# Kernel tuning notes

Hardware: AMD Instinct MI355X
Metric: run time of the kernel (lower is better)

Reference implementation:

```python
import jax, jax.numpy as jnp
import numpy as np

D_MODEL = 1024
NHEAD = 16
HEAD_DIM = D_MODEL // NHEAD
WINDOW = 256


def setup_inputs() -> dict:
    key = jax.random.key(0)
    kx, kq, kk, kv, ko = jax.random.split(key, 5)
    B, S = 2, 2048
    scale = 1.0 / np.sqrt(D_MODEL)
    x = jax.random.normal(kx, (B, S, D_MODEL), dtype=jnp.float32)
    Wq = jax.random.normal(kq, (D_MODEL, D_MODEL), dtype=jnp.float32) * scale
    Wk = jax.random.normal(kk, (D_MODEL, D_MODEL), dtype=jnp.float32) * scale
    Wv = jax.random.normal(kv, (D_MODEL, D_MODEL), dtype=jnp.float32) * scale
    Wo = jax.random.normal(ko, (D_MODEL, D_MODEL), dtype=jnp.float32) * scale
    return {"x": x, "Wq": Wq, "Wk": Wk, "Wv": Wv, "Wo": Wo}


def _sliding_window_mask(seq_len):
    # additive mask: 0 where (q - window + 1) <= k <= q, -inf elsewhere
    pos = jnp.arange(seq_len)
    qpos = pos[:, None]
    kpos = pos[None, :]
    valid = (kpos >= qpos - WINDOW + 1) & (kpos <= qpos)
    return jnp.where(valid, 0.0, -jnp.inf).astype(jnp.float32)


def reference(x, Wq, Wk, Wv, Wo):
    B, S, D = x.shape
    # projections (nn.Linear: x @ W.T; weights here stored as [out,in] equiv -> use x @ W.T)
    q = jnp.einsum('bsd,ed->bse', x, Wq)
    k = jnp.einsum('bsd,ed->bse', x, Wk)
    v = jnp.einsum('bsd,ed->bse', x, Wv)
    q = q.reshape(B, S, NHEAD, HEAD_DIM).transpose(0, 2, 1, 3)  # [B,H,S,Dh]
    k = k.reshape(B, S, NHEAD, HEAD_DIM).transpose(0, 2, 1, 3)
    v = v.reshape(B, S, NHEAD, HEAD_DIM).transpose(0, 2, 1, 3)
    mask = _sliding_window_mask(S)  # [S,S]
    scale = 1.0 / np.sqrt(HEAD_DIM)
    scores = jnp.einsum('bhqd,bhkd->bhqk', q, k) * scale + mask
    attn = jax.nn.softmax(scores, axis=-1)
    out = jnp.einsum('bhqk,bhkd->bhqd', attn, v)  # [B,H,S,Dh]
    out = out.transpose(0, 2, 1, 3).reshape(B, S, D)
    return jnp.einsum('bsd,ed->bse', out, Wo)
```

## Files before the change

### kernel.cpp

```cpp
#include <hip/hip_runtime.h>
#include <stdint.h>

#define S_LEN   2048
#define BATCH   2
#define DM      1024
#define NHEADS  16
#define HD      64
#define WIN     256
#define MROWS   (BATCH * S_LEN)
#define NX      (MROWS * DM)
#define NW      (DM * DM)

typedef unsigned short u16;
typedef unsigned int   u32;

using short8  = __attribute__((ext_vector_type(8))) short;
using floatx4 = __attribute__((ext_vector_type(4))) float;

__device__ __forceinline__ float bf2f(u16 u) {
    union { u32 u; float f; } v; v.u = ((u32)u) << 16; return v.f;
}
__device__ __forceinline__ u16 f2bf(float f) {
    union { float f; u32 u; } v; v.f = f;
    u32 u = v.u;
    u += 0x7fffu + ((u >> 16) & 1u);
    return (u16)(u >> 16);
}

__device__ __forceinline__ void load_lds16(const void* g, void* l) {
    __builtin_amdgcn_global_load_lds(
        (__attribute__((address_space(1))) void*)(uintptr_t)g,
        (__attribute__((address_space(3))) void*)(unsigned int)(uintptr_t)l,
        16, 0, 0);
}

__global__ __launch_bounds__(256) void normalize_inputs(
        const void* x, const void* wq, const void* wk, const void* wv, const void* wo,
        u16* xb, u16* wcat, u16* wob, int* flag) {
    __shared__ int sbad;
    if (threadIdx.x == 0) sbad = 0;
    __syncthreads();
    int bad = 0;
    for (int i = threadIdx.x; i < 4096; i += 256) {
        float v = bf2f(((const u16*)x)[i]);
        if (!(fabsf(v) < 1e6f)) bad = 1;
    }
    if (bad) atomicOr(&sbad, 1);
    __syncthreads();
    const int mode = sbad;
    if (blockIdx.x == 0 && threadIdx.x == 0) flag[0] = mode;
    if (mode == 0) return;
    const int total4 = (NX + 4 * NW) >> 2;
    for (int i4 = blockIdx.x * blockDim.x + threadIdx.x; i4 < total4;
         i4 += gridDim.x * blockDim.x) {
        const int i = i4 << 2;
        const float* src; u16* dst; int li;
        if (i < NX)              { src = (const float*)x;  dst = xb;          li = i; }
        else if (i < NX + NW)    { src = (const float*)wq; dst = wcat;        li = i - NX; }
        else if (i < NX + 2*NW)  { src = (const float*)wk; dst = wcat + NW;   li = i - NX - NW; }
        else if (i < NX + 3*NW)  { src = (const float*)wv; dst = wcat + 2*NW; li = i - NX - 2*NW; }
        else                     { src = (const float*)wo; dst = wob;         li = i - NX - 3*NW; }
        float4 v = *(const float4*)(src + li);
        ushort4 o;
        o.x = f2bf(v.x); o.y = f2bf(v.y); o.z = f2bf(v.z); o.w = f2bf(v.w);
        *(ushort4*)(dst + li) = o;
    }
}

#define BK 32
#define QSCALE 0.180336880f

template<int TBM, int TBN>
__global__ __launch_bounds__(256) void gemm_lds(
        const u16* __restrict__ Araw, const u16* __restrict__ Anorm,
        const u16* __restrict__ B0, const u16* __restrict__ B1,
        const u16* __restrict__ B2, const u16* __restrict__ Bnorm,
        void* __restrict__ C, u16* __restrict__ VT,
        int M, int N, int K,
        const int* __restrict__ flag, int final_out) {
    constexpr int NI = TBM / 32, NF = TBN / 32;
    __shared__ __align__(16) u16 sA[2][TBM * BK];
    __shared__ __align__(16) u16 sB[2][TBN * BK];

    const int mode = flag[0];
    const int tid  = threadIdx.x;
    const int lane = tid & 63, wave = tid >> 6;
    const int m0  = blockIdx.x * TBM;
    const int n0g = blockIdx.y * TBN;
    const int third = n0g >> 10;
    const u16* A = mode ? Anorm : Araw;
    const u16* B = mode ? (Bnorm + (size_t)third * NW)
                        : (third == 0 ? B0 : (third == 1 ? B1 : B2));
    const int n0 = n0g - third * 1024;

    const int srow = lane >> 2;
    const int scol = (lane & 3) * 8;
    const u16* gA = A + (size_t)(m0 + wave * 16 + srow) * K + scol;
    const u16* gB = B + (size_t)(n0 + wave * 16 + srow) * K + scol;
    const size_t rstep = (size_t)64 * K;
    const int lofs = wave * 16 * BK;

    const int n16 = lane & 15, quad = lane >> 4;
    const int m_off = (wave >> 1) * (TBM / 2), n_off = (wave & 1) * (TBN / 2);

    floatx4 acc[NI][NF] = {};
    const int NIT = K / BK;

    auto issue = [&](int k0, int buf) {
        #pragma unroll
        for (int ia = 0; ia < TBM / 64; ++ia)
            load_lds16(gA + k0 + ia * rstep, sA[buf] + lofs + ia * 64 * BK);
        #pragma unroll
        for (int ib = 0; ib < TBN / 64; ++ib)
            load_lds16(gB + k0 + ib * rstep, sB[buf] + lofs + ib * 64 * BK);
    };

    issue(0, 0);
    for (int it = 0; it < NIT; ++it) {
        const int cur = it & 1;
        __syncthreads();
        if (it + 1 < NIT) issue((it + 1) * BK, 1 - cur);
        short8 af[NI], bfr[NF];
        #pragma unroll
        for (int i = 0; i < NI; ++i)
            af[i] = *(const short8*)&sA[cur][(m_off + i * 16 + n16) * BK + quad * 8];
        #pragma unroll
        for (int j = 0; j < NF; ++j)
            bfr[j] = *(const short8*)&sB[cur][(n_off + j * 16 + n16) * BK + quad * 8];
        #pragma unroll
        for (int i = 0; i < NI; ++i) {
            #pragma unroll
            for (int j = 0; j < NF; ++j)
                acc[i][j] = __builtin_amdgcn_mfma_f32_16x16x32_bf16(
                    af[i], bfr[j], acc[i][j], 0, 0, 0);
        }
    }

    if (!final_out && n0g >= 2048) {
        #pragma unroll
        for (int i = 0; i < NI; ++i) {
            #pragma unroll
            for (int j = 0; j < NF; ++j) {
                int row = m0 + m_off + i * 16 + quad * 4;
                int b_ = row >> 11, s = row & 2047;
                int cv = (n0g - 2048) + n_off + j * 16 + n16;
                int h_ = cv >> 6, dl = cv & 63;
                u16 pack[4];
                #pragma unroll
                for (int r = 0; r < 4; ++r) pack[r] = f2bf(acc[i][j][r]);
                u16* dst = VT + (((size_t)(b_ * 16 + h_) * 64 + dl) * S_LEN + s);
                *(uint2*)dst = *(uint2*)pack;
            }
        }
        return;
    }
    const int outmode = final_out ? mode : 0;
    const float oscale = (!final_out && n0g < 1024) ? QSCALE : 1.0f;
    #pragma unroll
    for (int i = 0; i < NI; ++i) {
        #pragma unroll
        for (int j = 0; j < NF; ++j) {
            #pragma unroll
            for (int r = 0; r < 4; ++r) {
                int row = m0 + m_off + i * 16 + quad * 4 + r;
                int col = n0g + n_off + j * 16 + n16;
                size_t idx = (size_t)row * N + col;
                float v = acc[i][j][r] * oscale;
                if (outmode) ((float*)C)[idx] = v;
                else         ((u16*)C)[idx]   = f2bf(v);
            }
        }
    }
}

__global__ __launch_bounds__(256) void gemm_out(
        const u16* __restrict__ A,
        const u16* __restrict__ Braw,
        const u16* __restrict__ Bnorm,
        void* __restrict__ C,
        const int* __restrict__ flag) {
    __shared__ __align__(16) u16 sA[2][128 * 64];
    __shared__ __align__(16) u16 sB[2][64 * 64];

    const int mode = flag[0];
    const u16* B = mode ? Bnorm : Braw;
    const int tid  = threadIdx.x;
    const int lane = tid & 63, wave = tid >> 6;
    const int n16 = lane & 15, quad = lane >> 4;
    const int m0 = blockIdx.x * 128;
    const int n0 = blockIdx.y * 64;
    const int K = DM;

    const int srow = tid >> 3;
    const int scol = (tid & 7) * 8;
    const u16* gA = A + (size_t)(m0 + srow) * K + scol;
    const u16* gB = B + (size_t)(n0 + srow) * K + scol;
    const int lofs = wave * 512;

    auto issue = [&](int k0, int buf) {
        #pragma unroll
        for (int ia = 0; ia < 4; ++ia)
            load_lds16(gA + k0 + (size_t)ia * 32 * K, sA[buf] + ia * 2048 + lofs);
        #pragma unroll
        for (int ib = 0; ib < 2; ++ib)
            load_lds16(gB + k0 + (size_t)ib * 32 * K, sB[buf] + ib * 2048 + lofs);
    };

    const int m_off = (wave >> 1) * 64, n_off = (wave & 1) * 32;
    floatx4 acc[4][2] = {};

    issue(0, 0);
    for (int it = 0; it < 16; ++it) {
        const int cur = it & 1;
        __syncthreads();
        if (it + 1 < 16) issue((it + 1) * 64, 1 - cur);
        short8 a0[4], a1[4], b0[2], b1[2];
        #pragma unroll
        for (int i = 0; i < 4; ++i) {
            const int rb = (m_off + i * 16 + n16) * 64;
            a0[i] = *(const short8*)&sA[cur][rb + quad * 8];
            a1[i] = *(const short8*)&sA[cur][rb + 32 + quad * 8];
        }
        #pragma unroll
        for (int j = 0; j < 2; ++j) {
            const int rb = (n_off + j * 16 + n16) * 64;
            b0[j] = *(const short8*)&sB[cur][rb + quad * 8];
            b1[j] = *(const short8*)&sB[cur][rb + 32 + quad * 8];
        }
        #pragma unroll
        for (int i = 0; i < 4; ++i) {
            #pragma unroll
            for (int j = 0; j < 2; ++j)
                acc[i][j] = __builtin_amdgcn_mfma_f32_16x16x32_bf16(
                    a0[i], b0[j], acc[i][j], 0, 0, 0);
        }
        #pragma unroll
        for (int i = 0; i < 4; ++i) {
            #pragma unroll
            for (int j = 0; j < 2; ++j)
                acc[i][j] = __builtin_amdgcn_mfma_f32_16x16x32_bf16(
                    a1[i], b1[j], acc[i][j], 0, 0, 0);
        }
    }

    #pragma unroll
    for (int i = 0; i < 4; ++i) {
        #pragma unroll
        for (int j = 0; j < 2; ++j) {
            #pragma unroll
            for (int r = 0; r < 4; ++r) {
                int row = m0 + m_off + i * 16 + quad * 4 + r;
                int col = n0 + n_off + j * 16 + n16;
                size_t idx = (size_t)row * DM + col;
                float v = acc[i][j][r];
                if (mode) ((float*)C)[idx] = v;
                else      ((u16*)C)[idx]   = f2bf(v);
            }
        }
    }
}

#define NCHUNK 10

__global__ __launch_bounds__(256) void attn_mfma(
        const u16* __restrict__ QKV, const u16* __restrict__ VT,
        u16* __restrict__ O) {
    __shared__ __align__(16) u16 sK[2][32][72];
    __shared__ __align__(16) u16 sVt[2][64][40];
    __shared__ __align__(16) u16 sP[4][2][16][40];

    const int bh = blockIdx.x;
    const int b  = bh >> 4, h = bh & 15;
    const int q0 = blockIdx.y * 64;
    const int ks0 = q0 - 256;
    const int tid = threadIdx.x;
    const u16* base = QKV + (size_t)b * S_LEN * 3072;
    const u16* Kb = base + 1024 + h * 64;
    const u16* Vb = VT + (size_t)bh * 64 * S_LEN;

    const int kRow = tid >> 3;
    const int kSeg = tid & 7;
    const int vD   = tid >> 2;
    const int vSeg = tid & 3;

    auto issue_loads = [&](int c, uint4& kv, uint4& vv) {
        const int ks = ks0 + c * 32;
        int kg = ks + kRow;
        uint4 k0 = {0u, 0u, 0u, 0u};
        if (kg >= 0 && kg < S_LEN)
            k0 = *(const uint4*)(Kb + (size_t)kg * 3072 + kSeg * 8);
        kv = k0;
        int vk = ks + vSeg * 8;
        uint4 v0 = {0u, 0u, 0u, 0u};
        if (vk >= 0 && vk + 8 <= S_LEN)
            v0 = *(const uint4*)(Vb + (size_t)vD * S_LEN + vk);
        vv = v0;
    };
    auto write_lds = [&](int buf, const uint4& kv, const uint4& vv) {
        *(uint4*)&sK[buf][kRow][kSeg * 8] = kv;
        *(uint4*)&sVt[buf][vD][vSeg * 8] = vv;
    };

    const int wave = tid >> 6, lane = tid & 63;
    const int n16 = lane & 15, quad = lane >> 4;
    const int sqb = q0 + wave * 16;
    const int sq_r0 = sqb + quad * 4;
    const int cfirst = wave >> 1;

    const u16* qrow = base + (size_t)(sqb + n16) * 3072 + h * 64;
    short8 aq0 = *(const short8*)(qrow + quad * 8);
    short8 aq1 = *(const short8*)(qrow + 32 + quad * 8);

    floatx4 o0 = {0.f,0.f,0.f,0.f}, o1 = o0, o2 = o0, o3 = o0;
    float lsum[4] = {0.f, 0.f, 0.f, 0.f};

    uint4 kvA, vvA, kvB, vvB;
    issue_loads(0, kvA, vvA);
    issue_loads(1, kvB, vvB);
    write_lds(0, kvA, vvA);

    for (int c = 0; c < NCHUNK; ++c) {
        const int buf = c & 1;
        __syncthreads();
        if (c + 2 < NCHUNK) {
            if ((c & 1) == 0) issue_loads(c + 2, kvA, vvA);
            else              issue_loads(c + 2, kvB, vvB);
        }
        if (c + 1 < NCHUNK) {
            if ((c & 1) == 0) write_lds(1 - buf, kvB, vvB);
            else              write_lds(1 - buf, kvA, vvA);
        }
        if (c < cfirst || c > cfirst + 8) continue;

        short8 bk00 = *(const short8*)&sK[buf][n16][quad * 8];
        short8 bk01 = *(const short8*)&sK[buf][n16][32 + quad * 8];
        short8 bk10 = *(const short8*)&sK[buf][16 + n16][quad * 8];
        short8 bk11 = *(const short8*)&sK[buf][16 + n16][32 + quad * 8];
        floatx4 z = {0.f, 0.f, 0.f, 0.f};
        __builtin_amdgcn_s_setprio(1);
        floatx4 s0 = __builtin_amdgcn_mfma_f32_16x16x32_bf16(aq0, bk00, z, 0, 0, 0);
        s0 = __builtin_amdgcn_mfma_f32_16x16x32_bf16(aq1, bk01, s0, 0, 0, 0);
        floatx4 s1 = __builtin_amdgcn_mfma_f32_16x16x32_bf16(aq0, bk10, z, 0, 0, 0);
        s1 = __builtin_amdgcn_mfma_f32_16x16x32_bf16(aq1, bk11, s1, 0, 0, 0);
        __builtin_amdgcn_s_setprio(0);

        const int kg0 = ks0 + c * 32 + n16;
        const int kg1 = kg0 + 16;
        float p0[4], p1[4];
        #pragma unroll
        for (int r = 0; r < 4; ++r) {
            int sq = sq_r0 + r;
            int lo = sq - (WIN - 1); if (lo < 0) lo = 0;
            float v0 = (kg0 >= lo && kg0 <= sq) ? s0[r] : -3e38f;
            float v1 = (kg1 >= lo && kg1 <= sq) ? s1[r] : -3e38f;
            p0[r] = exp2f(v0);
            p1[r] = exp2f(v1);
            lsum[r] += p0[r] + p1[r];
        }
        u16* pw = &sP[wave][c & 1][0][0];
        #pragma unroll
        for (int r = 0; r < 4; ++r) {
            pw[(quad * 4 + r) * 40 + n16]      = f2bf(p0[r]);
            pw[(quad * 4 + r) * 40 + 16 + n16] = f2bf(p1[r]);
        }
        asm volatile("s_waitcnt lgkmcnt(0)" ::: "memory");
        short8 pa  = *(const short8*)&pw[n16 * 40 + quad * 8];
        short8 bv0 = *(const short8*)&sVt[buf][n16]     [quad * 8];
        short8 bv1 = *(const short8*)&sVt[buf][16 + n16][quad * 8];
        short8 bv2 = *(const short8*)&sVt[buf][32 + n16][quad * 8];
        short8 bv3 = *(const short8*)&sVt[buf][48 + n16][quad * 8];
        __builtin_amdgcn_s_setprio(1);
        o0 = __builtin_amdgcn_mfma_f32_16x16x32_bf16(pa, bv0, o0, 0, 0, 0);
        o1 = __builtin_amdgcn_mfma_f32_16x16x32_bf16(pa, bv1, o1, 0, 0, 0);
        o2 = __builtin_amdgcn_mfma_f32_16x16x32_bf16(pa, bv2, o2, 0, 0, 0);
        o3 = __builtin_amdgcn_mfma_f32_16x16x32_bf16(pa, bv3, o3, 0, 0, 0);
        __builtin_amdgcn_s_setprio(0);
    }

    #pragma unroll
    for (int r = 0; r < 4; ++r) {
        float s = lsum[r];
        s += __shfl_xor(s, 1);
        s += __shfl_xor(s, 2);
        s += __shfl_xor(s, 4);
        s += __shfl_xor(s, 8);
        lsum[r] = s;
    }

    #pragma unroll
    for (int r = 0; r < 4; ++r) {
        float rl = 1.0f / lsum[r];
        size_t ro = ((size_t)(b * S_LEN + sq_r0 + r)) * DM + h * 64 + n16;
        O[ro]      = f2bf(o0[r] * rl);
        O[ro + 16] = f2bf(o1[r] * rl);
        O[ro + 32] = f2bf(o2[r] * rl);
        O[ro + 48] = f2bf(o3[r] * rl);
    }
}

extern "C" void kernel_launch(void* const* d_in, const int* in_sizes, int n_in,
                              void* d_out, int out_size, void* d_ws, size_t ws_size,
                              hipStream_t stream) {
    char* ws = (char*)d_ws;
    int* flag = (int*)ws;
    u16* xb   = (u16*)(ws + 1024);
    u16* wcat = xb   + (size_t)NX;
    u16* wob  = wcat + (size_t)3 * NW;
    u16* qkv  = wob  + (size_t)NW;
    u16* ob   = qkv  + (size_t)MROWS * 3 * DM;
    u16* vt   = ob   + (size_t)NX;

    const u16* xr  = (const u16*)d_in[0];
    const u16* wqr = (const u16*)d_in[1];
    const u16* wkr = (const u16*)d_in[2];
    const u16* wvr = (const u16*)d_in[3];
    const u16* wor = (const u16*)d_in[4];

    normalize_inputs<<<1024, 256, 0, stream>>>(
        d_in[0], d_in[1], d_in[2], d_in[3], d_in[4], xb, wcat, wob, flag);
    gemm_lds<128, 128><<<dim3(MROWS / 128, 3072 / 128), 256, 0, stream>>>(
        xr, xb, wqr, wkr, wvr, wcat, qkv, vt, MROWS, 3 * DM, DM, flag, 0);
    attn_mfma<<<dim3(BATCH * NHEADS, S_LEN / 64), 256, 0, stream>>>(qkv, vt, ob);
    gemm_out<<<dim3(MROWS / 128, DM / 64), 256, 0, stream>>>(
        ob, wor, wob, d_out, flag);
}
```

Baseline: 154.6 us.

## Double attention KV chunk size to 64 keys and halve loop iterations

The sliding-window attention kernel now processes 64 keys per chunk instead of 32, giving 5 chunks instead of 10, with larger K/V LDS tiles and a single per-wave P buffer. This halves the number of block barriers and load/store phases and gives more MFMA work per sync. In exchange, every wave now computes all chunks rather than skipping those outside its window. That adds some redundant masked work, and the larger LDS footprint may reduce occupancy.

Result: no change. 155.0 us (+0.3%).

```diff
diff --git a/kernel.cpp b/kernel.cpp
--- a/kernel.cpp
+++ b/kernel.cpp
@@ -260,14 +260,14 @@
     }
 }
 
-#define NCHUNK 10
+#define NCHUNK 5
 
 __global__ __launch_bounds__(256) void attn_mfma(
         const u16* __restrict__ QKV, const u16* __restrict__ VT,
         u16* __restrict__ O) {
-    __shared__ __align__(16) u16 sK[2][32][72];
-    __shared__ __align__(16) u16 sVt[2][64][40];
-    __shared__ __align__(16) u16 sP[4][2][16][40];
+    __shared__ __align__(16) u16 sK[2][64][72];
+    __shared__ __align__(16) u16 sVt[2][64][72];
+    __shared__ __align__(16) u16 sP[4][16][72];
 
     const int bh = blockIdx.x;
     const int b  = bh >> 4, h = bh & 15;
@@ -283,29 +283,35 @@
     const int vD   = tid >> 2;
     const int vSeg = tid & 3;
 
-    auto issue_loads = [&](int c, uint4& kv, uint4& vv) {
-        const int ks = ks0 + c * 32;
-        int kg = ks + kRow;
-        uint4 k0 = {0u, 0u, 0u, 0u};
-        if (kg >= 0 && kg < S_LEN)
-            k0 = *(const uint4*)(Kb + (size_t)kg * 3072 + kSeg * 8);
-        kv = k0;
-        int vk = ks + vSeg * 8;
-        uint4 v0 = {0u, 0u, 0u, 0u};
-        if (vk >= 0 && vk + 8 <= S_LEN)
-            v0 = *(const uint4*)(Vb + (size_t)vD * S_LEN + vk);
-        vv = v0;
+    auto issue_loads = [&](int c, uint4& k0v, uint4& k1v, uint4& v0v, uint4& v1v) {
+        const int ks = ks0 + c * 64;
+        int kg0 = ks + kRow, kg1 = kg0 + 32;
+        uint4 t0 = {0u,0u,0u,0u}, t1 = {0u,0u,0u,0u};
+        if (kg0 >= 0 && kg0 < S_LEN)
+            t0 = *(const uint4*)(Kb + (size_t)kg0 * 3072 + kSeg * 8);
+        if (kg1 >= 0 && kg1 < S_LEN)
+            t1 = *(const uint4*)(Kb + (size_t)kg1 * 3072 + kSeg * 8);
+        k0v = t0; k1v = t1;
+        int vk0 = ks + vSeg * 8, vk1 = vk0 + 32;
+        uint4 u0 = {0u,0u,0u,0u}, u1 = {0u,0u,0u,0u};
+        if (vk0 >= 0 && vk0 + 8 <= S_LEN)
+            u0 = *(const uint4*)(Vb + (size_t)vD * S_LEN + vk0);
+        if (vk1 >= 0 && vk1 + 8 <= S_LEN)
+            u1 = *(const uint4*)(Vb + (size_t)vD * S_LEN + vk1);
+        v0v = u0; v1v = u1;
     };
-    auto write_lds = [&](int buf, const uint4& kv, const uint4& vv) {
-        *(uint4*)&sK[buf][kRow][kSeg * 8] = kv;
-        *(uint4*)&sVt[buf][vD][vSeg * 8] = vv;
+    auto write_lds = [&](int buf, const uint4& k0v, const uint4& k1v,
+                         const uint4& v0v, const uint4& v1v) {
+        *(uint4*)&sK[buf][kRow][kSeg * 8]      = k0v;
+        *(uint4*)&sK[buf][kRow + 32][kSeg * 8] = k1v;
+        *(uint4*)&sVt[buf][vD][vSeg * 8]       = v0v;
+        *(uint4*)&sVt[buf][vD][32 + vSeg * 8]  = v1v;
     };
 
     const int wave = tid >> 6, lane = tid & 63;
     const int n16 = lane & 15, quad = lane >> 4;
     const int sqb = q0 + wave * 16;
     const int sq_r0 = sqb + quad * 4;
-    const int cfirst = wave >> 1;
 
     const u16* qrow = base + (size_t)(sqb + n16) * 3072 + h * 64;
     short8 aq0 = *(const short8*)(qrow + quad * 8);
@@ -314,66 +320,87 @@
     floatx4 o0 = {0.f,0.f,0.f,0.f}, o1 = o0, o2 = o0, o3 = o0;
     float lsum[4] = {0.f, 0.f, 0.f, 0.f};
 
-    uint4 kvA, vvA, kvB, vvB;
-    issue_loads(0, kvA, vvA);
-    issue_loads(1, kvB, vvB);
-    write_lds(0, kvA, vvA);
+    uint4 kA0, kA1, vA0, vA1, kB0, kB1, vB0, vB1;
+    issue_loads(0, kA0, kA1, vA0, vA1);
+    issue_loads(1, kB0, kB1, vB0, vB1);
+    write_lds(0, kA0, kA1, vA0, vA1);
 
     for (int c = 0; c < NCHUNK; ++c) {
         const int buf = c & 1;
         __syncthreads();
         if (c + 2 < NCHUNK) {
-            if ((c & 1) == 0) issue_loads(c + 2, kvA, vvA);
-            else              issue_loads(c + 2, kvB, vvB);
+            if ((c & 1) == 0) issue_loads(c + 2, kA0, kA1, vA0, vA1);
+            else              issue_loads(c + 2, kB0, kB1, vB0, vB1);
         }
         if (c + 1 < NCHUNK) {
-            if ((c & 1) == 0) write_lds(1 - buf, kvB, vvB);
-            else              write_lds(1 - buf, kvA, vvA);
-        }
-        if (c < cfirst || c > cfirst + 8) continue;
-
-        short8 bk00 = *(const short8*)&sK[buf][n16][quad * 8];
-        short8 bk01 = *(const short8*)&sK[buf][n16][32 + quad * 8];
-        short8 bk10 = *(const short8*)&sK[buf][16 + n16][quad * 8];
-        short8 bk11 = *(const short8*)&sK[buf][16 + n16][32 + quad * 8];
-        floatx4 z = {0.f, 0.f, 0.f, 0.f};
-        __builtin_amdgcn_s_setprio(1);
-        floatx4 s0 = __builtin_amdgcn_mfma_f32_16x16x32_bf16(aq0, bk00, z, 0, 0, 0);
-        s0 = __builtin_amdgcn_mfma_f32_16x16x32_bf16(aq1, bk01, s0, 0, 0, 0);
-        floatx4 s1 = __builtin_amdgcn_mfma_f32_16x16x32_bf16(aq0, bk10, z, 0, 0, 0);
-        s1 = __builtin_amdgcn_mfma_f32_16x16x32_bf16(aq1, bk11, s1, 0, 0, 0);
-        __builtin_amdgcn_s_setprio(0);
-
-        const int kg0 = ks0 + c * 32 + n16;
-        const int kg1 = kg0 + 16;
-        float p0[4], p1[4];
+            if ((c & 1) == 0) write_lds(1 - buf, kB0, kB1, vB0, vB1);
+            else              write_lds(1 - buf, kA0, kA1, vA0, vA1);
+        }
+
+        floatx4 s0, s1, s2, s3;
+        {
+            const floatx4 z = {0.f, 0.f, 0.f, 0.f};
+            __builtin_amdgcn_s_setprio(1);
+            short8 bk;
+            bk = *(const short8*)&sK[buf][n16][quad * 8];
+            s0 = __builtin_amdgcn_mfma_f32_16x16x32_bf16(aq0, bk, z, 0, 0, 0);
+            bk = *(const short8*)&sK[buf][n16][32 + quad * 8];
+            s0 = __builtin_amdgcn_mfma_f32_16x16x32_bf16(aq1, bk, s0, 0, 0, 0);
+            bk = *(const short8*)&sK[buf][16 + n16][quad * 8];
+            s1 = __builtin_amdgcn_mfma_f32_16x16x32_bf16(aq0, bk, z, 0, 0, 0);
+            bk = *(const short8*)&sK[buf][16 + n16][32 + quad * 8];
+            s1 = __builtin_amdgcn_mfma_f32_16x16x32_bf16(aq1, bk, s1, 0, 0, 0);
+            bk = *(const short8*)&sK[buf][32 + n16][quad * 8];
+            s2 = __builtin_amdgcn_mfma_f32_16x16x32_bf16(aq0, bk, z, 0, 0, 0);
+            bk = *(const short8*)&sK[buf][32 + n16][32 + quad * 8];
+            s2 = __builtin_amdgcn_mfma_f32_16x16x32_bf16(aq1, bk, s2, 0, 0, 0);
+            bk = *(const short8*)&sK[buf][48 + n16][quad * 8];
+            s3 = __builtin_amdgcn_mfma_f32_16x16x32_bf16(aq0, bk, z, 0, 0, 0);
+            bk = *(const short8*)&sK[buf][48 + n16][32 + quad * 8];
+            s3 = __builtin_amdgcn_mfma_f32_16x16x32_bf16(aq1, bk, s3, 0, 0, 0);
+            __builtin_amdgcn_s_setprio(0);
+        }
+
+        u16* pw = &sP[wave][0][0];
+        const int kgb = ks0 + c * 64 + n16;
         #pragma unroll
         for (int r = 0; r < 4; ++r) {
             int sq = sq_r0 + r;
             int lo = sq - (WIN - 1); if (lo < 0) lo = 0;
-            float v0 = (kg0 >= lo && kg0 <= sq) ? s0[r] : -3e38f;
-            float v1 = (kg1 >= lo && kg1 <= sq) ? s1[r] : -3e38f;
-            p0[r] = exp2f(v0);
-            p1[r] = exp2f(v1);
-            lsum[r] += p0[r] + p1[r];
-        }
-        u16* pw = &sP[wave][c & 1][0][0];
-        #pragma unroll
-        for (int r = 0; r < 4; ++r) {
-            pw[(quad * 4 + r) * 40 + n16]      = f2bf(p0[r]);
-            pw[(quad * 4 + r) * 40 + 16 + n16] = f2bf(p1[r]);
+            float p;
+            p = exp2f((kgb      >= lo && kgb      <= sq) ? s0[r] : -3e38f);
+            lsum[r] += p; pw[(quad * 4 + r) * 72 + n16]      = f2bf(p);
+            p = exp2f((kgb + 16 >= lo && kgb + 16 <= sq) ? s1[r] : -3e38f);
+            lsum[r] += p; pw[(quad * 4 + r) * 72 + 16 + n16] = f2bf(p);
+            p = exp2f((kgb + 32 >= lo && kgb + 32 <= sq) ? s2[r] : -3e38f);
+            lsum[r] += p; pw[(quad * 4 + r) * 72 + 32 + n16] = f2bf(p);
+            p = exp2f((kgb + 48 >= lo && kgb + 48 <= sq) ? s3[r] : -3e38f);
+            lsum[r] += p; pw[(quad * 4 + r) * 72 + 48 + n16] = f2bf(p);
         }
         asm volatile("s_waitcnt lgkmcnt(0)" ::: "memory");
-        short8 pa  = *(const short8*)&pw[n16 * 40 + quad * 8];
-        short8 bv0 = *(const short8*)&sVt[buf][n16]     [quad * 8];
-        short8 bv1 = *(const short8*)&sVt[buf][16 + n16][quad * 8];
-        short8 bv2 = *(const short8*)&sVt[buf][32 + n16][quad * 8];
-        short8 bv3 = *(const short8*)&sVt[buf][48 + n16][quad * 8];
+
+        short8 pa0 = *(const short8*)&pw[n16 * 72 + quad * 8];
+        short8 pa1 = *(const short8*)&pw[n16 * 72 + 32 + quad * 8];
         __builtin_amdgcn_s_setprio(1);
-        o0 = __builtin_amdgcn_mfma_f32_16x16x32_bf16(pa, bv0, o0, 0, 0, 0);
-        o1 = __builtin_amdgcn_mfma_f32_16x16x32_bf16(pa, bv1, o1, 0, 0, 0);
-        o2 = __builtin_amdgcn_mfma_f32_16x16x32_bf16(pa, bv2, o2, 0, 0, 0);
-        o3 = __builtin_amdgcn_mfma_f32_16x16x32_bf16(pa, bv3, o3, 0, 0, 0);
+        {
+            short8 bv;
+            bv = *(const short8*)&sVt[buf][n16][quad * 8];
+            o0 = __builtin_amdgcn_mfma_f32_16x16x32_bf16(pa0, bv, o0, 0, 0, 0);
+            bv = *(const short8*)&sVt[buf][n16][32 + quad * 8];
+            o0 = __builtin_amdgcn_mfma_f32_16x16x32_bf16(pa1, bv, o0, 0, 0, 0);
+            bv = *(const short8*)&sVt[buf][16 + n16][quad * 8];
+            o1 = __builtin_amdgcn_mfma_f32_16x16x32_bf16(pa0, bv, o1, 0, 0, 0);
+            bv = *(const short8*)&sVt[buf][16 + n16][32 + quad * 8];
+            o1 = __builtin_amdgcn_mfma_f32_16x16x32_bf16(pa1, bv, o1, 0, 0, 0);
+            bv = *(const short8*)&sVt[buf][32 + n16][quad * 8];
+            o2 = __builtin_amdgcn_mfma_f32_16x16x32_bf16(pa0, bv, o2, 0, 0, 0);
+            bv = *(const short8*)&sVt[buf][32 + n16][32 + quad * 8];
+            o2 = __builtin_amdgcn_mfma_f32_16x16x32_bf16(pa1, bv, o2, 0, 0, 0);
+            bv = *(const short8*)&sVt[buf][48 + n16][quad * 8];
+            o3 = __builtin_amdgcn_mfma_f32_16x16x32_bf16(pa0, bv, o3, 0, 0, 0);
+            bv = *(const short8*)&sVt[buf][48 + n16][32 + quad * 8];
+            o3 = __builtin_amdgcn_mfma_f32_16x16x32_bf16(pa1, bv, o3, 0, 0, 0);
+        }
         __builtin_amdgcn_s_setprio(0);
     }
 
```
